# Optimization experiments

Measured on AMD Instinct MI355X. Metric: run time of the kernel, lower is better.

## Reference

```python
import jax, jax.numpy as jnp
import numpy as np

B, N, C, NH = 8, 16384, 256, 8
CH = C // NH          # head dim = 32
SCALE = CH ** -0.5
HH = WW = 128         # N = HH*WW
# CoaT crpe window dict {3:2, 5:3, 7:3}: 2 heads->3x3, 3 heads->5x5, 3 heads->7x7


def setup_inputs() -> dict:
    key = jax.random.key(0)
    ks = jax.random.split(key, 9)
    w = lambda k, shp: (jax.random.normal(k, shp, jnp.float32) * 0.02)
    return {
        "x": jax.random.normal(ks[0], (B, N, C), jnp.float32),
        "w_qkv": w(ks[1], (C, 3 * C)),              # qkv_bias=False
        "w_proj": w(ks[2], (C, C)),
        "b_proj": jnp.zeros((C,), jnp.float32),
        "w3": w(ks[3], (3, 3, 1, 2 * CH)),          # HWIO depthwise, 2 heads
        "b3": jnp.zeros((2 * CH,), jnp.float32),
        "w5": w(ks[4], (5, 5, 1, 3 * CH)),          # 3 heads
        "b5": jnp.zeros((3 * CH,), jnp.float32),
        "w7": w(ks[5], (7, 7, 1, 3 * CH)),          # 3 heads
        "b7": jnp.zeros((3 * CH,), jnp.float32),
        "H": HH,
        "W": WW,
    }


def _hydra(q, k, v):
    # q,k,v: [B, h, N, Ch]; normalize over feature dim, O(N) token reduction
    qn = q * jax.lax.rsqrt(jnp.sum(q * q, axis=-1, keepdims=True))
    kn = k * jax.lax.rsqrt(jnp.sum(k * k, axis=-1, keepdims=True))
    kv = jnp.sum(kn * v, axis=-2, keepdims=True)   # [B, h, 1, Ch]
    return qn * kv                                  # broadcast over tokens


def _dwconv(img, kern, bias):
    # img: [B, c, H, W]; kern: [kh, kw, 1, c] (HWIO depthwise)
    c = img.shape[1]
    out = jax.lax.conv_general_dilated(
        img, kern, window_strides=(1, 1), padding="SAME",
        feature_group_count=c,
        dimension_numbers=("NCHW", "HWIO", "NCHW"))
    return out + bias[None, :, None, None]


def _crpe(q, v, Hs, Ws, convs):
    # CoaT ConvRelPosEnc: depthwise conv on v per head group, gated by q
    b, h, n, ch = v.shape
    outs, idx = [], 0
    for heads, kern, bias in convs:
        vs = v[:, idx:idx + heads]                          # [B, hs, N, Ch]
        v_img = vs.transpose(0, 1, 3, 2).reshape(b, heads * ch, Hs, Ws)
        cv = _dwconv(v_img, kern, bias)
        cv = cv.reshape(b, heads, ch, n).transpose(0, 1, 3, 2)
        outs.append(q[:, idx:idx + heads] * cv)
        idx += heads
    return jnp.concatenate(outs, axis=1)                    # [B, h, N, Ch]


def reference(x, w_qkv, w_proj, b_proj, w3, b3, w5, b5, w7, b7, H, W):
    b, n, c = x.shape
    qkv = (x @ w_qkv).reshape(b, n, 3, NH, CH).transpose(2, 0, 3, 1, 4)
    q, k, v = qkv[0], qkv[1], qkv[2]                        # [B, h, N, Ch]
    factor_att = _hydra(q, k, v)
    crpe = _crpe(q, v, H, W, [(2, w3, b3), (3, w5, b5), (3, w7, b7)])
    out = SCALE * factor_att + crpe
    out = out.transpose(0, 2, 1, 3).reshape(b, n, c)        # [B, N, C]
    return out @ w_proj + b_proj
```

## Files before the change

kernel.cpp:

```cpp
#include <hip/hip_runtime.h>
#include <hip/hip_bf16.h>


typedef __hip_bfloat16 bf16;
typedef __bf16 bf16x8 __attribute__((ext_vector_type(8)));
typedef unsigned short u16x8 __attribute__((ext_vector_type(8)));
typedef float f32x4 __attribute__((ext_vector_type(4)));
typedef float f32x8 __attribute__((ext_vector_type(8)));

#define SCALE_ 0.17677669529663687f

__device__ __forceinline__ unsigned short f2b(float f) {
  __hip_bfloat16 h = __float2bfloat16(f);
  return __builtin_bit_cast(unsigned short, h);
}
__device__ __forceinline__ float blo(unsigned u) {
  return __builtin_bit_cast(float, u << 16);
}
__device__ __forceinline__ float bhi(unsigned u) {
  return __builtin_bit_cast(float, u & 0xffff0000u);
}
__device__ __forceinline__ f32x8 unpack8(uint4 u) {
  f32x8 r;
  r[0] = blo(u.x); r[1] = bhi(u.x); r[2] = blo(u.y); r[3] = bhi(u.y);
  r[4] = blo(u.z); r[5] = bhi(u.z); r[6] = blo(u.w); r[7] = bhi(u.w);
  return r;
}
__device__ __forceinline__ uint4 pack8v(const f32x8 o) {
  uint4 s;
  s.x = (unsigned)f2b(o[0]) | ((unsigned)f2b(o[1]) << 16);
  s.y = (unsigned)f2b(o[2]) | ((unsigned)f2b(o[3]) << 16);
  s.z = (unsigned)f2b(o[4]) | ((unsigned)f2b(o[5]) << 16);
  s.w = (unsigned)f2b(o[6]) | ((unsigned)f2b(o[7]) << 16);
  return s;
}
__device__ __forceinline__ void gload16(const void* g, void* l) {
  __builtin_amdgcn_global_load_lds(
      (const __attribute__((address_space(1))) unsigned int*)g,
      (__attribute__((address_space(3))) unsigned int*)l, 16, 0, 0);
}
__device__ __forceinline__ f32x4 mfma16(u16x8 a, u16x8 b, f32x4 c) {
  return __builtin_amdgcn_mfma_f32_16x16x32_bf16(
      __builtin_bit_cast(bf16x8, a), __builtin_bit_cast(bf16x8, b), c, 0, 0, 0);
}
__device__ __forceinline__ void barrier_vm4() {
  asm volatile("s_waitcnt vmcnt(4) lgkmcnt(0)" ::: "memory");
  __builtin_amdgcn_s_barrier();
  asm volatile("" ::: "memory");
}
__device__ __forceinline__ void barrier_vm0() {
  asm volatile("s_waitcnt vmcnt(0) lgkmcnt(0)" ::: "memory");
  __builtin_amdgcn_s_barrier();
  asm volatile("" ::: "memory");
}
__device__ __forceinline__ void barrier_vm8() {
  asm volatile("s_waitcnt vmcnt(8) lgkmcnt(0)" ::: "memory");
  __builtin_amdgcn_s_barrier();
  asm volatile("" ::: "memory");
}
__device__ __forceinline__ void fma8(f32x8& a, const f32x8 v, const float4 w0,
                                     const float4 w1) {
  a[0] += v[0] * w0.x; a[1] += v[1] * w0.y;
  a[2] += v[2] * w0.z; a[3] += v[3] * w0.w;
  a[4] += v[4] * w1.x; a[5] += v[5] * w1.y;
  a[6] += v[6] * w1.z; a[7] += v[7] * w1.w;
}

__global__ __launch_bounds__(256) void prep_weights(
    const float* __restrict__ wqkv, const float* __restrict__ wproj,
    bf16* __restrict__ wqkvT, bf16* __restrict__ wprojT) {
  const int idx = blockIdx.x * 256 + threadIdx.x;
  if (idx < 768 * 256) {
    const int j = idx >> 8, k = idx & 255;
    wqkvT[idx] = __float2bfloat16(wqkv[k * 768 + j]);
  }
  if (idx < 256 * 256) {
    const int j = idx >> 8, k = idx & 255;
    wprojT[idx] = __float2bfloat16(wproj[k * 256 + j]);
  }
}

__global__ __launch_bounds__(256) void qkv_mfma(
    const float* __restrict__ x, const bf16* __restrict__ wT,
    bf16* __restrict__ qO, bf16* __restrict__ kO, bf16* __restrict__ vO) {
  __shared__ __align__(16) char LDSU[32768];
  char* As = LDSU;
  char* Bs = LDSU + 16384;
  const int tid = threadIdx.x;
  const int l = tid & 63, w = tid >> 6;
  const int wr = w >> 1, wc = w & 1;

  const int lin = blockIdx.y * 6 + blockIdx.x;
  const int xcd = lin & 7, qq = lin >> 3;
  const int jt = qq % 6;
  const int ttile = xcd * 128 + qq / 6;
  const int j0 = jt << 7;
  const int t0 = ttile << 7;

  f32x4 acc[4][4];
#pragma unroll
  for (int m = 0; m < 4; ++m)
#pragma unroll
    for (int t = 0; t < 4; ++t) acc[m][t] = (f32x4){0.f, 0.f, 0.f, 0.f};

  const int arow0 = w * 16 + (l >> 2), arow1 = arow0 + 64;
  const int asl = l & 3;
  const bf16* asrc0 =
      wT + (size_t)(j0 + arow0) * 256 + ((asl ^ ((arow0 >> 1) & 3)) << 3);
  const bf16* asrc1 =
      wT + (size_t)(j0 + arow1) * 256 + ((asl ^ ((arow1 >> 1) & 3)) << 3);
  const int ad0 = w * 1024, ad1 = 4096 + w * 1024;

  const int brow = tid >> 1, bkh = tid & 1;
  const float* xp = x + (size_t)(t0 + brow) * 256 + bkh * 16;
  const int bsw = (brow >> 1) & 3;
  const int bw0 = brow * 64 + (((bkh << 1) ^ bsw) << 4);
  const int bw1 = brow * 64 + ((((bkh << 1) | 1) ^ bsw) << 4);

  const int fr = l & 15;
  const int fq = l >> 4;
  const int fs = (fq ^ ((l >> 1) & 3)) << 4;

  float4 xs[3][4];

  gload16(asrc0, As + ad0);
  gload16(asrc1, As + ad1);
#pragma unroll
  for (int s = 0; s < 3; ++s)
#pragma unroll
    for (int i = 0; i < 4; ++i)
      xs[s][i] = *(const float4*)(xp + s * 32 + i * 4);
  {
    u16x8 p0, p1;
    p0[0] = f2b(xs[0][0].x); p0[1] = f2b(xs[0][0].y);
    p0[2] = f2b(xs[0][0].z); p0[3] = f2b(xs[0][0].w);
    p0[4] = f2b(xs[0][1].x); p0[5] = f2b(xs[0][1].y);
    p0[6] = f2b(xs[0][1].z); p0[7] = f2b(xs[0][1].w);
    p1[0] = f2b(xs[0][2].x); p1[1] = f2b(xs[0][2].y);
    p1[2] = f2b(xs[0][2].z); p1[3] = f2b(xs[0][2].w);
    p1[4] = f2b(xs[0][3].x); p1[5] = f2b(xs[0][3].y);
    p1[6] = f2b(xs[0][3].z); p1[7] = f2b(xs[0][3].w);
    *(u16x8*)(Bs + bw0) = p0;
    *(u16x8*)(Bs + bw1) = p1;
  }
  barrier_vm8();

#pragma unroll
  for (int t = 0; t < 8; ++t) {
    if (t < 7) {
      const int kn = (t + 1) << 5;
      char* Adst = As + (((t + 1) & 1) << 13);
      gload16(asrc0 + kn, Adst + ad0);
      gload16(asrc1 + kn, Adst + ad1);
    }
    if (t < 5) {
#pragma unroll
      for (int i = 0; i < 4; ++i)
        xs[t % 3][i] = *(const float4*)(xp + (t + 3) * 32 + i * 4);
    }
    const char* Ac = As + ((t & 1) << 13);
    const char* Bc = Bs + ((t & 1) << 13);
    u16x8 af[4], bfv[4];
#pragma unroll
    for (int m = 0; m < 4; ++m)
      af[m] = *(const u16x8*)(Ac + (wr * 64 + m * 16 + fr) * 64 + fs);
#pragma unroll
    for (int tt = 0; tt < 4; ++tt)
      bfv[tt] = *(const u16x8*)(Bc + (wc * 64 + tt * 16 + fr) * 64 + fs);
    __builtin_amdgcn_s_setprio(1);
#pragma unroll
    for (int m = 0; m < 4; ++m)
#pragma unroll
      for (int tt = 0; tt < 4; ++tt)
        acc[m][tt] = mfma16(af[m], bfv[tt], acc[m][tt]);
    __builtin_amdgcn_s_setprio(0);
    if (t < 7) {
      const float4* xv = xs[(t + 1) % 3];
      u16x8 p0, p1;
      p0[0] = f2b(xv[0].x); p0[1] = f2b(xv[0].y);
      p0[2] = f2b(xv[0].z); p0[3] = f2b(xv[0].w);
      p0[4] = f2b(xv[1].x); p0[5] = f2b(xv[1].y);
      p0[6] = f2b(xv[1].z); p0[7] = f2b(xv[1].w);
      p1[0] = f2b(xv[2].x); p1[1] = f2b(xv[2].y);
      p1[2] = f2b(xv[2].z); p1[3] = f2b(xv[2].w);
      p1[4] = f2b(xv[3].x); p1[5] = f2b(xv[3].y);
      p1[6] = f2b(xv[3].z); p1[7] = f2b(xv[3].w);
      char* Bdst = Bs + (((t + 1) & 1) << 13);
      *(u16x8*)(Bdst + bw0) = p0;
      *(u16x8*)(Bdst + bw1) = p1;
    }
    if (t < 5) barrier_vm4();
    else if (t < 7) barrier_vm0();
  }
  __syncthreads();

#pragma unroll
  for (int m = 0; m < 4; ++m) {
    const int jq = wr * 16 + m * 4 + fq;
#pragma unroll
    for (int t = 0; t < 4; ++t) {
      const int token = wc * 64 + t * 16 + fr;
      const int p = jq ^ (token & 15);
      uint2 pk;
      pk.x = (unsigned)f2b(acc[m][t][0]) | ((unsigned)f2b(acc[m][t][1]) << 16);
      pk.y = (unsigned)f2b(acc[m][t][2]) | ((unsigned)f2b(acc[m][t][3]) << 16);
      *(uint2*)(LDSU + token * 256 + (p << 3)) = pk;
    }
  }
  __syncthreads();

  const int region = j0 >> 8;
  bf16* outp = (region == 0) ? qO : ((region == 1) ? kO : vO);
  const int b = t0 >> 14;
  const int n0 = t0 & 16383;
  const int jl = j0 & 255;
  const int seg = tid & 15;
#pragma unroll
  for (int r = 0; r < 8; ++r) {
    const int token = r * 16 + (tid >> 4);
    const int tsw = token & 15;
    const uint2 lo = *(const uint2*)(LDSU + token * 256 + (((2 * seg) ^ tsw) << 3));
    const uint2 hi =
        *(const uint2*)(LDSU + token * 256 + (((2 * seg + 1) ^ tsw) << 3));
    uint4 d;
    d.x = lo.x; d.y = lo.y; d.z = hi.x; d.w = hi.y;
    *(uint4*)&outp[((size_t)b * 16384 + n0 + token) * 256 + jl + seg * 8] = d;
  }
}

__global__ __launch_bounds__(256) void kv_reduce(
    const bf16* __restrict__ kT, const bf16* __restrict__ vT,
    float* __restrict__ kv) {
  __shared__ float red[256 * 8];
  const int tid = threadIdx.x;
  const int b = blockIdx.y;
  const int seg = tid & 31;
  f32x8 part = (f32x8)0.f;

  for (int r = 0; r < 32; ++r) {
    const int token = blockIdx.x * 256 + r * 8 + (tid >> 5);
    const size_t roff = ((size_t)b * 16384 + token) * 256;
    const uint4 kd = *(const uint4*)(kT + roff + seg * 8);
    const f32x8 kf = unpack8(kd);
    float ss = 0.f;
#pragma unroll
    for (int i = 0; i < 8; ++i) ss += kf[i] * kf[i];
    ss += __shfl_xor(ss, 1);
    ss += __shfl_xor(ss, 2);
    const float inv = rsqrtf(ss);
    const uint4 vd = *(const uint4*)(vT + roff + seg * 8);
    const f32x8 vf = unpack8(vd);
#pragma unroll
    for (int i = 0; i < 8; ++i) part[i] += kf[i] * inv * vf[i];
  }
#pragma unroll
  for (int i = 0; i < 8; ++i) red[tid * 8 + i] = part[i];
  __syncthreads();
  if (tid < 32) {
    f32x8 s = (f32x8)0.f;
#pragma unroll
    for (int k = 0; k < 8; ++k)
#pragma unroll
      for (int i = 0; i < 8; ++i) s[i] += red[(tid + 32 * k) * 8 + i];
#pragma unroll
    for (int i = 0; i < 8; ++i)
      atomicAdd(&kv[b * 256 + seg * 8 + i], s[i]);
  }
}

template <int K>
__global__ __launch_bounds__(256) void crpe_conv(
    const bf16* __restrict__ qT, const bf16* __restrict__ vT,
    const float* __restrict__ kvbuf, const float* __restrict__ wp,
    const float* __restrict__ bp, int OC, int hbase,
    bf16* __restrict__ mid) {
  constexpr int R = K / 2;
  constexpr int SY = 16 + 2 * R;
  constexpr int SXr = 32 + 2 * R;
  constexpr int SX = SXr + 1;
  constexpr int PL = SX * SY;
  __shared__ __align__(16) uint4 vs[4 * PL];
  __shared__ float wlds[K * K * 32];
  __shared__ float blds[32];

  const int tid = threadIdx.x;
  const int hg = blockIdx.x;
  const int h = hbase + hg;
  const int tile = blockIdx.y;
  const int b = blockIdx.z;
  const int tx0 = (tile & 3) * 32, ty0 = (tile >> 2) * 16;
  const int tx = tid & 15, ty = tid >> 4;
  const int ocbase = hg * 32;

  {
    const int cc = tid & 3;
    for (int e = tid >> 2; e < SXr * SY; e += 64) {
      const int ly = e / SXr, lx = e - ly * SXr;
      const int gy = ty0 - R + ly, gx = tx0 - R + lx;
      uint4 d = {0, 0, 0, 0};
      if (gy >= 0 && gy < 128 && gx >= 0 && gx < 128)
        d = *((const uint4*)(vT + ((size_t)b * 16384 + gy * 128 + gx) * 256 +
                             h * 32) + cc);
      vs[cc * PL + ly * SX + lx] = d;
    }
  }
  for (int e = tid; e < K * K * 32; e += 256)
    wlds[e] = wp[(e >> 5) * OC + ocbase + (e & 31)];
  if (tid < 32) blds[tid] = bp[ocbase + tid];
  __syncthreads();

  const int n = (ty0 + ty) * 128 + tx0 + 2 * tx;
  const size_t off0 = ((size_t)b * 16384 + n) * 256 + h * 32;
  const uint4* q0 = (const uint4*)(qT + off0);
  const uint4* q1 = (const uint4*)(qT + off0 + 256);
  float ss0 = 0.f, ss1 = 0.f;
#pragma unroll
  for (int cc = 0; cc < 4; ++cc) {
    const f32x8 a = unpack8(q0[cc]);
    const f32x8 c = unpack8(q1[cc]);
#pragma unroll
    for (int i = 0; i < 8; ++i) { ss0 += a[i] * a[i]; ss1 += c[i] * c[i]; }
  }
  const float qinv0 = rsqrtf(ss0), qinv1 = rsqrtf(ss1);
  const float4* kvp = (const float4*)(kvbuf + ((size_t)b * 8 + h) * 32);
  const float4* wlds4 = (const float4*)wlds;
  const float4* bl4 = (const float4*)blds;
  uint4* m0 = (uint4*)(mid + off0);
  uint4* m1 = (uint4*)(mid + off0 + 256);

#pragma unroll 1
  for (int cc = 0; cc < 4; ++cc) {
    const uint4* vplane = vs + cc * PL;
    const float4 ba = bl4[cc * 2], bb = bl4[cc * 2 + 1];
    f32x8 a0, a1;
    a0[0] = ba.x; a0[1] = ba.y; a0[2] = ba.z; a0[3] = ba.w;
    a0[4] = bb.x; a0[5] = bb.y; a0[6] = bb.z; a0[7] = bb.w;
    a1 = a0;
#pragma unroll
    for (int ky = 0; ky < K; ++ky) {
      const uint4* vrow = vplane + (ty + ky) * SX + 2 * tx;
      f32x8 vcur = unpack8(vrow[0]);
#pragma unroll
      for (int kx = 0; kx < K; ++kx) {
        const f32x8 vnx = unpack8(vrow[kx + 1]);
        const float4 w0 = wlds4[(ky * K + kx) * 8 + cc * 2];
        const float4 w1 = wlds4[(ky * K + kx) * 8 + cc * 2 + 1];
        fma8(a0, vcur, w0, w1);
        fma8(a1, vnx, w0, w1);
        vcur = vnx;
      }
    }
    const float4 ka = kvp[cc * 2], kb = kvp[cc * 2 + 1];
    f32x8 kvf;
    kvf[0] = ka.x; kvf[1] = ka.y; kvf[2] = ka.z; kvf[3] = ka.w;
    kvf[4] = kb.x; kvf[5] = kb.y; kvf[6] = kb.z; kvf[7] = kb.w;
    {
      const f32x8 qv = unpack8(q0[cc]);
      f32x8 o;
#pragma unroll
      for (int i = 0; i < 8; ++i)
        o[i] = SCALE_ * qv[i] * qinv0 * kvf[i] + qv[i] * a0[i];
      m0[cc] = pack8v(o);
    }
    {
      const f32x8 qv = unpack8(q1[cc]);
      f32x8 o;
#pragma unroll
      for (int i = 0; i < 8; ++i)
        o[i] = SCALE_ * qv[i] * qinv1 * kvf[i] + qv[i] * a1[i];
      m1[cc] = pack8v(o);
    }
  }
}

__global__ __launch_bounds__(256) void proj_mfma(
    const bf16* __restrict__ mid, const bf16* __restrict__ wpT,
    const float* __restrict__ bproj, float* __restrict__ out) {
  __shared__ __align__(16) char LDSU[49152];
  char* As = LDSU;
  char* Bs = LDSU + 24576;
  const int tid = threadIdx.x;
  const int l = tid & 63, w = tid >> 6;
  const int wr = w >> 1, wc = w & 1;

  const int lin = blockIdx.y * 2 + blockIdx.x;
  const int xcd = lin & 7, qq = lin >> 3;
  const int jt = qq & 1;
  const int ttile = xcd * 128 + (qq >> 1);
  const int j0 = jt << 7;
  const int tk0 = ttile << 7;

  f32x4 acc[4][4];
#pragma unroll
  for (int m = 0; m < 4; ++m)
#pragma unroll
    for (int t = 0; t < 4; ++t) acc[m][t] = (f32x4){0.f, 0.f, 0.f, 0.f};

  const int row0 = w * 16 + (l >> 2), row1 = row0 + 64;
  const int sl = l & 3;
  const int sw0 = (row0 >> 1) & 3, sw1 = (row1 >> 1) & 3;
  const bf16* asrc0 = wpT + (size_t)(j0 + row0) * 256 + ((sl ^ sw0) << 3);
  const bf16* asrc1 = wpT + (size_t)(j0 + row1) * 256 + ((sl ^ sw1) << 3);
  const bf16* bsrc0 = mid + (size_t)(tk0 + row0) * 256 + ((sl ^ sw0) << 3);
  const bf16* bsrc1 = mid + (size_t)(tk0 + row1) * 256 + ((sl ^ sw1) << 3);
  const int d0 = w * 1024, d1 = 4096 + w * 1024;

  const int fr = l & 15;
  const int fq = l >> 4;
  const int fs = (fq ^ ((l >> 1) & 3)) << 4;

  gload16(asrc0, As + d0);
  gload16(asrc1, As + d1);
  gload16(bsrc0, Bs + d0);
  gload16(bsrc1, Bs + d1);
  gload16(asrc0 + 32, As + 8192 + d0);
  gload16(asrc1 + 32, As + 8192 + d1);
  gload16(bsrc0 + 32, Bs + 8192 + d0);
  gload16(bsrc1 + 32, Bs + 8192 + d1);
  barrier_vm4();

#pragma unroll
  for (int t = 0; t < 8; ++t) {
    if (t < 6) {
      const int kn = (t + 2) << 5;
      const int nb = ((t + 2) % 3) * 8192;
      gload16(asrc0 + kn, As + nb + d0);
      gload16(asrc1 + kn, As + nb + d1);
      gload16(bsrc0 + kn, Bs + nb + d0);
      gload16(bsrc1 + kn, Bs + nb + d1);
    }
    const char* Ac = As + (t % 3) * 8192;
    const char* Bc = Bs + (t % 3) * 8192;
    u16x8 af[4], bfv[4];
#pragma unroll
    for (int m = 0; m < 4; ++m)
      af[m] = *(const u16x8*)(Ac + (wr * 64 + m * 16 + fr) * 64 + fs);
#pragma unroll
    for (int tt = 0; tt < 4; ++tt)
      bfv[tt] = *(const u16x8*)(Bc + (wc * 64 + tt * 16 + fr) * 64 + fs);
    __builtin_amdgcn_s_setprio(1);
#pragma unroll
    for (int m = 0; m < 4; ++m)
#pragma unroll
      for (int tt = 0; tt < 4; ++tt)
        acc[m][tt] = mfma16(af[m], bfv[tt], acc[m][tt]);
    __builtin_amdgcn_s_setprio(0);
    if (t < 6) barrier_vm4();
    else if (t < 7) barrier_vm0();
  }
  __syncthreads();

#pragma unroll
  for (int m = 0; m < 4; ++m) {
    const float4 bias = *(const float4*)&bproj[j0 + wr * 64 + m * 16 + fq * 4];
#pragma unroll
    for (int t = 0; t < 4; ++t) {
      acc[m][t][0] += bias.x;
      acc[m][t][1] += bias.y;
      acc[m][t][2] += bias.z;
      acc[m][t][3] += bias.w;
    }
  }

  for (int chunk = 0; chunk < 2; ++chunk) {
    if (wc == chunk) {
#pragma unroll
      for (int m = 0; m < 4; ++m) {
        const int jq = wr * 16 + m * 4 + fq;
#pragma unroll
        for (int t = 0; t < 4; ++t) {
          const int ltok = t * 16 + fr;
          const int p = jq ^ (ltok & 15);
          float4 r;
          r.x = acc[m][t][0]; r.y = acc[m][t][1];
          r.z = acc[m][t][2]; r.w = acc[m][t][3];
          *(float4*)(LDSU + ltok * 512 + (p << 4)) = r;
        }
      }
    }
    __syncthreads();
    const int seg = tid & 31;
#pragma unroll
    for (int r = 0; r < 8; ++r) {
      const int ltok = r * 8 + (tid >> 5);
      const int p = seg ^ (ltok & 15);
      const float4 dv = *(const float4*)(LDSU + ltok * 512 + (p << 4));
      *(float4*)&out[(size_t)(tk0 + chunk * 64 + ltok) * 256 + j0 + seg * 4] = dv;
    }
    __syncthreads();
  }
}

extern "C" void kernel_launch(void* const* d_in, const int* in_sizes, int n_in,
                              void* d_out, int out_size, void* d_ws,
                              size_t ws_size, hipStream_t stream) {
  const float* x     = (const float*)d_in[0];
  const float* wqkv  = (const float*)d_in[1];
  const float* wproj = (const float*)d_in[2];
  const float* bproj = (const float*)d_in[3];
  const float* w3 = (const float*)d_in[4];
  const float* b3 = (const float*)d_in[5];
  const float* w5 = (const float*)d_in[6];
  const float* b5 = (const float*)d_in[7];
  const float* w7 = (const float*)d_in[8];
  const float* b7 = (const float*)d_in[9];
  float* out = (float*)d_out;

  const size_t PLANE = (size_t)8 * 16384 * 256;
  bf16* qT  = (bf16*)d_ws;
  bf16* vT  = qT + PLANE;
  bf16* kT  = vT + PLANE;
  bf16* mid = kT;
  float* kv = (float*)(kT + PLANE);
  bf16* wqkvT  = (bf16*)(kv + 2048);
  bf16* wprojT = wqkvT + 768 * 256;

  hipMemsetAsync(kv, 0, 2048 * sizeof(float), stream);
  prep_weights<<<dim3(768), 256, 0, stream>>>(wqkv, wproj, wqkvT, wprojT);
  qkv_mfma<<<dim3(6, 1024), 256, 0, stream>>>(x, wqkvT, qT, kT, vT);
  kv_reduce<<<dim3(64, 8), 256, 0, stream>>>(kT, vT, kv);
  crpe_conv<3><<<dim3(2, 32, 8), 256, 0, stream>>>(qT, vT, kv, w3, b3, 64, 0, mid);
  crpe_conv<5><<<dim3(3, 32, 8), 256, 0, stream>>>(qT, vT, kv, w5, b5, 96, 2, mid);
  crpe_conv<7><<<dim3(3, 32, 8), 256, 0, stream>>>(qT, vT, kv, w7, b7, 96, 5, mid);
  proj_mfma<<<dim3(2, 1024), 256, 0, stream>>>(mid, wprojT, bproj, out);
}
```

Measured before the change: 381.7 us.

## Stage full activation tile in LDS, stream weights into registers, drop per-step barriers

Both the QKV and projection GEMM kernels now load the whole 128-token x 256-K activation tile into a 64KB swizzled LDS buffer up front, with an fp32-to-bf16 conversion pass in qkv and a global_load_lds copy in proj. Weight fragments are read straight from global memory into registers with a 3-deep register ring. This removes the per-K-step LDS double buffering and the barriers between steps. The projection epilogue is also changed to write all 128 tokens through LDS in a single pass instead of two chunks. The cost is 64KB of LDS per block, which lowers occupancy. Weight reads from global are also less coalesced, and the kernel no longer overlaps activation loading with MFMA work.

```diff
diff --git a/kernel.cpp b/kernel.cpp
--- a/kernel.cpp
+++ b/kernel.cpp
@@ -43,21 +43,6 @@
   return __builtin_amdgcn_mfma_f32_16x16x32_bf16(
       __builtin_bit_cast(bf16x8, a), __builtin_bit_cast(bf16x8, b), c, 0, 0, 0);
 }
-__device__ __forceinline__ void barrier_vm4() {
-  asm volatile("s_waitcnt vmcnt(4) lgkmcnt(0)" ::: "memory");
-  __builtin_amdgcn_s_barrier();
-  asm volatile("" ::: "memory");
-}
-__device__ __forceinline__ void barrier_vm0() {
-  asm volatile("s_waitcnt vmcnt(0) lgkmcnt(0)" ::: "memory");
-  __builtin_amdgcn_s_barrier();
-  asm volatile("" ::: "memory");
-}
-__device__ __forceinline__ void barrier_vm8() {
-  asm volatile("s_waitcnt vmcnt(8) lgkmcnt(0)" ::: "memory");
-  __builtin_amdgcn_s_barrier();
-  asm volatile("" ::: "memory");
-}
 __device__ __forceinline__ void fma8(f32x8& a, const f32x8 v, const float4 w0,
                                      const float4 w1) {
   a[0] += v[0] * w0.x; a[1] += v[1] * w0.y;
@@ -83,9 +68,7 @@
 __global__ __launch_bounds__(256) void qkv_mfma(
     const float* __restrict__ x, const bf16* __restrict__ wT,
     bf16* __restrict__ qO, bf16* __restrict__ kO, bf16* __restrict__ vO) {
-  __shared__ __align__(16) char LDSU[32768];
-  char* As = LDSU;
-  char* Bs = LDSU + 16384;
+  __shared__ __align__(16) char XL[65536];
   const int tid = threadIdx.x;
   const int l = tid & 63, w = tid >> 6;
   const int wr = w >> 1, wc = w & 1;
@@ -96,101 +79,71 @@
   const int ttile = xcd * 128 + qq / 6;
   const int j0 = jt << 7;
   const int t0 = ttile << 7;
-
-  f32x4 acc[4][4];
-#pragma unroll
-  for (int m = 0; m < 4; ++m)
-#pragma unroll
-    for (int t = 0; t < 4; ++t) acc[m][t] = (f32x4){0.f, 0.f, 0.f, 0.f};
-
-  const int arow0 = w * 16 + (l >> 2), arow1 = arow0 + 64;
-  const int asl = l & 3;
-  const bf16* asrc0 =
-      wT + (size_t)(j0 + arow0) * 256 + ((asl ^ ((arow0 >> 1) & 3)) << 3);
-  const bf16* asrc1 =
-      wT + (size_t)(j0 + arow1) * 256 + ((asl ^ ((arow1 >> 1) & 3)) << 3);
-  const int ad0 = w * 1024, ad1 = 4096 + w * 1024;
-
-  const int brow = tid >> 1, bkh = tid & 1;
-  const float* xp = x + (size_t)(t0 + brow) * 256 + bkh * 16;
-  const int bsw = (brow >> 1) & 3;
-  const int bw0 = brow * 64 + (((bkh << 1) ^ bsw) << 4);
-  const int bw1 = brow * 64 + ((((bkh << 1) | 1) ^ bsw) << 4);
+  const int b = t0 >> 14;
+  const int n0 = t0 & 16383;
+
+  {
+    const int tk = tid >> 5, s = tid & 31;
+#pragma unroll 4
+    for (int r = 0; r < 16; ++r) {
+      const int row = r * 8 + tk;
+      const float4 a0 = *(const float4*)(x + (size_t)(t0 + row) * 256 + s * 8);
+      const float4 a1 =
+          *(const float4*)(x + (size_t)(t0 + row) * 256 + s * 8 + 4);
+      u16x8 p;
+      p[0] = f2b(a0.x); p[1] = f2b(a0.y); p[2] = f2b(a0.z); p[3] = f2b(a0.w);
+      p[4] = f2b(a1.x); p[5] = f2b(a1.y); p[6] = f2b(a1.z); p[7] = f2b(a1.w);
+      *(u16x8*)(XL + row * 512 + ((s ^ (row & 7)) << 4)) = p;
+    }
+  }
 
   const int fr = l & 15;
   const int fq = l >> 4;
-  const int fs = (fq ^ ((l >> 1) & 3)) << 4;
-
-  float4 xs[3][4];
-
-  gload16(asrc0, As + ad0);
-  gload16(asrc1, As + ad1);
-#pragma unroll
-  for (int s = 0; s < 3; ++s)
-#pragma unroll
-    for (int i = 0; i < 4; ++i)
-      xs[s][i] = *(const float4*)(xp + s * 32 + i * 4);
-  {
-    u16x8 p0, p1;
-    p0[0] = f2b(xs[0][0].x); p0[1] = f2b(xs[0][0].y);
-    p0[2] = f2b(xs[0][0].z); p0[3] = f2b(xs[0][0].w);
-    p0[4] = f2b(xs[0][1].x); p0[5] = f2b(xs[0][1].y);
-    p0[6] = f2b(xs[0][1].z); p0[7] = f2b(xs[0][1].w);
-    p1[0] = f2b(xs[0][2].x); p1[1] = f2b(xs[0][2].y);
-    p1[2] = f2b(xs[0][2].z); p1[3] = f2b(xs[0][2].w);
-    p1[4] = f2b(xs[0][3].x); p1[5] = f2b(xs[0][3].y);
-    p1[6] = f2b(xs[0][3].z); p1[7] = f2b(xs[0][3].w);
-    *(u16x8*)(Bs + bw0) = p0;
-    *(u16x8*)(Bs + bw1) = p1;
-  }
-  barrier_vm8();
+
+  const bf16* abase = wT + (size_t)(j0 + wr * 64 + fr) * 256 + fq * 8;
+
+  int btok[4], btsw[4];
+#pragma unroll
+  for (int tt = 0; tt < 4; ++tt) {
+    btok[tt] = wc * 64 + tt * 16 + fr;
+    btsw[tt] = btok[tt] & 7;
+  }
+
+  f32x4 acc[4][4];
+#pragma unroll
+  for (int m = 0; m < 4; ++m)
+#pragma unroll
+    for (int t = 0; t < 4; ++t) acc[m][t] = (f32x4){0.f, 0.f, 0.f, 0.f};
+
+  u16x8 wreg[3][4];
+#pragma unroll
+  for (int s = 0; s < 2; ++s)
+#pragma unroll
+    for (int m = 0; m < 4; ++m)
+      wreg[s][m] = *(const u16x8*)(abase + m * 4096 + s * 32);
+
+  __syncthreads();
 
 #pragma unroll
   for (int t = 0; t < 8; ++t) {
-    if (t < 7) {
-      const int kn = (t + 1) << 5;
-      char* Adst = As + (((t + 1) & 1) << 13);
-      gload16(asrc0 + kn, Adst + ad0);
-      gload16(asrc1 + kn, Adst + ad1);
-    }
-    if (t < 5) {
-#pragma unroll
-      for (int i = 0; i < 4; ++i)
-        xs[t % 3][i] = *(const float4*)(xp + (t + 3) * 32 + i * 4);
-    }
-    const char* Ac = As + ((t & 1) << 13);
-    const char* Bc = Bs + ((t & 1) << 13);
-    u16x8 af[4], bfv[4];
+    if (t < 6) {
+#pragma unroll
+      for (int m = 0; m < 4; ++m)
+        wreg[(t + 2) % 3][m] =
+            *(const u16x8*)(abase + m * 4096 + (t + 2) * 32);
+    }
+    u16x8 bfv[4];
+#pragma unroll
+    for (int tt = 0; tt < 4; ++tt)
+      bfv[tt] = *(const u16x8*)(XL + btok[tt] * 512 +
+                                (((4 * t + fq) ^ btsw[tt]) << 4));
+    __builtin_amdgcn_s_setprio(1);
 #pragma unroll
     for (int m = 0; m < 4; ++m)
-      af[m] = *(const u16x8*)(Ac + (wr * 64 + m * 16 + fr) * 64 + fs);
-#pragma unroll
-    for (int tt = 0; tt < 4; ++tt)
-      bfv[tt] = *(const u16x8*)(Bc + (wc * 64 + tt * 16 + fr) * 64 + fs);
-    __builtin_amdgcn_s_setprio(1);
-#pragma unroll
-    for (int m = 0; m < 4; ++m)
 #pragma unroll
       for (int tt = 0; tt < 4; ++tt)
-        acc[m][tt] = mfma16(af[m], bfv[tt], acc[m][tt]);
+        acc[m][tt] = mfma16(wreg[t % 3][m], bfv[tt], acc[m][tt]);
     __builtin_amdgcn_s_setprio(0);
-    if (t < 7) {
-      const float4* xv = xs[(t + 1) % 3];
-      u16x8 p0, p1;
-      p0[0] = f2b(xv[0].x); p0[1] = f2b(xv[0].y);
-      p0[2] = f2b(xv[0].z); p0[3] = f2b(xv[0].w);
-      p0[4] = f2b(xv[1].x); p0[5] = f2b(xv[1].y);
-      p0[6] = f2b(xv[1].z); p0[7] = f2b(xv[1].w);
-      p1[0] = f2b(xv[2].x); p1[1] = f2b(xv[2].y);
-      p1[2] = f2b(xv[2].z); p1[3] = f2b(xv[2].w);
-      p1[4] = f2b(xv[3].x); p1[5] = f2b(xv[3].y);
-      p1[6] = f2b(xv[3].z); p1[7] = f2b(xv[3].w);
-      char* Bdst = Bs + (((t + 1) & 1) << 13);
-      *(u16x8*)(Bdst + bw0) = p0;
-      *(u16x8*)(Bdst + bw1) = p1;
-    }
-    if (t < 5) barrier_vm4();
-    else if (t < 7) barrier_vm0();
   }
   __syncthreads();
 
@@ -204,24 +157,22 @@
       uint2 pk;
       pk.x = (unsigned)f2b(acc[m][t][0]) | ((unsigned)f2b(acc[m][t][1]) << 16);
       pk.y = (unsigned)f2b(acc[m][t][2]) | ((unsigned)f2b(acc[m][t][3]) << 16);
-      *(uint2*)(LDSU + token * 256 + (p << 3)) = pk;
+      *(uint2*)(XL + token * 256 + (p << 3)) = pk;
     }
   }
   __syncthreads();
 
   const int region = j0 >> 8;
   bf16* outp = (region == 0) ? qO : ((region == 1) ? kO : vO);
-  const int b = t0 >> 14;
-  const int n0 = t0 & 16383;
   const int jl = j0 & 255;
   const int seg = tid & 15;
 #pragma unroll
   for (int r = 0; r < 8; ++r) {
     const int token = r * 16 + (tid >> 4);
     const int tsw = token & 15;
-    const uint2 lo = *(const uint2*)(LDSU + token * 256 + (((2 * seg) ^ tsw) << 3));
+    const uint2 lo = *(const uint2*)(XL + token * 256 + (((2 * seg) ^ tsw) << 3));
     const uint2 hi =
-        *(const uint2*)(LDSU + token * 256 + (((2 * seg + 1) ^ tsw) << 3));
+        *(const uint2*)(XL + token * 256 + (((2 * seg + 1) ^ tsw) << 3));
     uint4 d;
     d.x = lo.x; d.y = lo.y; d.z = hi.x; d.w = hi.y;
     *(uint4*)&outp[((size_t)b * 16384 + n0 + token) * 256 + jl + seg * 8] = d;
@@ -376,9 +327,7 @@
 __global__ __launch_bounds__(256) void proj_mfma(
     const bf16* __restrict__ mid, const bf16* __restrict__ wpT,
     const float* __restrict__ bproj, float* __restrict__ out) {
-  __shared__ __align__(16) char LDSU[49152];
-  char* As = LDSU;
-  char* Bs = LDSU + 24576;
+  __shared__ __align__(16) char XL[65536];
   const int tid = threadIdx.x;
   const int l = tid & 63, w = tid >> 6;
   const int wr = w >> 1, wc = w & 1;
@@ -389,66 +338,68 @@
   const int ttile = xcd * 128 + (qq >> 1);
   const int j0 = jt << 7;
   const int tk0 = ttile << 7;
-
-  f32x4 acc[4][4];
-#pragma unroll
-  for (int m = 0; m < 4; ++m)
-#pragma unroll
-    for (int t = 0; t < 4; ++t) acc[m][t] = (f32x4){0.f, 0.f, 0.f, 0.f};
-
-  const int row0 = w * 16 + (l >> 2), row1 = row0 + 64;
-  const int sl = l & 3;
-  const int sw0 = (row0 >> 1) & 3, sw1 = (row1 >> 1) & 3;
-  const bf16* asrc0 = wpT + (size_t)(j0 + row0) * 256 + ((sl ^ sw0) << 3);
-  const bf16* asrc1 = wpT + (size_t)(j0 + row1) * 256 + ((sl ^ sw1) << 3);
-  const bf16* bsrc0 = mid + (size_t)(tk0 + row0) * 256 + ((sl ^ sw0) << 3);
-  const bf16* bsrc1 = mid + (size_t)(tk0 + row1) * 256 + ((sl ^ sw1) << 3);
-  const int d0 = w * 1024, d1 = 4096 + w * 1024;
+  const int b = tk0 >> 14;
+  const int n0 = tk0 & 16383;
+
+  {
+    const int ltk = l >> 5;
+    const int s = l & 31;
+#pragma unroll 4
+    for (int i = 0; i < 16; ++i) {
+      const int shot_tok = w * 32 + i * 2;
+      const int tok = shot_tok + ltk;
+      gload16(mid + ((size_t)b * 16384 + n0 + tok) * 256 + ((s ^ (tok & 7)) << 3),
+              XL + shot_tok * 512);
+    }
+  }
 
   const int fr = l & 15;
   const int fq = l >> 4;
-  const int fs = (fq ^ ((l >> 1) & 3)) << 4;
-
-  gload16(asrc0, As + d0);
-  gload16(asrc1, As + d1);
-  gload16(bsrc0, Bs + d0);
-  gload16(bsrc1, Bs + d1);
-  gload16(asrc0 + 32, As + 8192 + d0);
-  gload16(asrc1 + 32, As + 8192 + d1);
-  gload16(bsrc0 + 32, Bs + 8192 + d0);
-  gload16(bsrc1 + 32, Bs + 8192 + d1);
-  barrier_vm4();
+  const bf16* abase = wpT + (size_t)(j0 + wr * 64 + fr) * 256 + fq * 8;
+
+  int btok[4], btsw[4];
+#pragma unroll
+  for (int tt = 0; tt < 4; ++tt) {
+    btok[tt] = wc * 64 + tt * 16 + fr;
+    btsw[tt] = btok[tt] & 7;
+  }
+
+  f32x4 acc[4][4];
+#pragma unroll
+  for (int m = 0; m < 4; ++m)
+#pragma unroll
+    for (int t = 0; t < 4; ++t) acc[m][t] = (f32x4){0.f, 0.f, 0.f, 0.f};
+
+  u16x8 wreg[3][4];
+#pragma unroll
+  for (int s = 0; s < 2; ++s)
+#pragma unroll
+    for (int m = 0; m < 4; ++m)
+      wreg[s][m] = *(const u16x8*)(abase + m * 4096 + s * 32);
+
+  __syncthreads();
 
 #pragma unroll
   for (int t = 0; t < 8; ++t) {
     if (t < 6) {
-      const int kn = (t + 2) << 5;
-      const int nb = ((t + 2) % 3) * 8192;
-      gload16(asrc0 + kn, As + nb + d0);
-      gload16(asrc1 + kn, As + nb + d1);
-      gload16(bsrc0 + kn, Bs + nb + d0);
-      gload16(bsrc1 + kn, Bs + nb + d1);
-    }
-    const char* Ac = As + (t % 3) * 8192;
-    const char* Bc = Bs + (t % 3) * 8192;
-    u16x8 af[4], bfv[4];
+#pragma unroll
+      for (int m = 0; m < 4; ++m)
+        wreg[(t + 2) % 3][m] =
+            *(const u16x8*)(abase + m * 4096 + (t + 2) * 32);
+    }
+    u16x8 bfv[4];
+#pragma unroll
+    for (int tt = 0; tt < 4; ++tt)
+      bfv[tt] = *(const u16x8*)(XL + btok[tt] * 512 +
+                                (((4 * t + fq) ^ btsw[tt]) << 4));
+    __builtin_amdgcn_s_setprio(1);
 #pragma unroll
     for (int m = 0; m < 4; ++m)
-      af[m] = *(const u16x8*)(Ac + (wr * 64 + m * 16 + fr) * 64 + fs);
-#pragma unroll
-    for (int tt = 0; tt < 4; ++tt)
-      bfv[tt] = *(const u16x8*)(Bc + (wc * 64 + tt * 16 + fr) * 64 + fs);
-    __builtin_amdgcn_s_setprio(1);
-#pragma unroll
-    for (int m = 0; m < 4; ++m)
 #pragma unroll
       for (int tt = 0; tt < 4; ++tt)
-        acc[m][tt] = mfma16(af[m], bfv[tt], acc[m][tt]);
+        acc[m][tt] = mfma16(wreg[t % 3][m], bfv[tt], acc[m][tt]);
     __builtin_amdgcn_s_setprio(0);
-    if (t < 6) barrier_vm4();
-    else if (t < 7) barrier_vm0();
-  }
-  __syncthreads();
+  }
 
 #pragma unroll
   for (int m = 0; m < 4; ++m) {
@@ -461,33 +412,29 @@
       acc[m][t][3] += bias.w;
     }
   }
-
-  for (int chunk = 0; chunk < 2; ++chunk) {
-    if (wc == chunk) {
-#pragma unroll
-      for (int m = 0; m < 4; ++m) {
-        const int jq = wr * 16 + m * 4 + fq;
-#pragma unroll
-        for (int t = 0; t < 4; ++t) {
-          const int ltok = t * 16 + fr;
-          const int p = jq ^ (ltok & 15);
-          float4 r;
-          r.x = acc[m][t][0]; r.y = acc[m][t][1];
-          r.z = acc[m][t][2]; r.w = acc[m][t][3];
-          *(float4*)(LDSU + ltok * 512 + (p << 4)) = r;
-        }
-      }
-    }
-    __syncthreads();
-    const int seg = tid & 31;
-#pragma unroll
-    for (int r = 0; r < 8; ++r) {
-      const int ltok = r * 8 + (tid >> 5);
-      const int p = seg ^ (ltok & 15);
-      const float4 dv = *(const float4*)(LDSU + ltok * 512 + (p << 4));
-      *(float4*)&out[(size_t)(tk0 + chunk * 64 + ltok) * 256 + j0 + seg * 4] = dv;
-    }
-    __syncthreads();
+  __syncthreads();
+
+#pragma unroll
+  for (int m = 0; m < 4; ++m) {
+    const int jq = wr * 16 + m * 4 + fq;
+#pragma unroll
+    for (int t = 0; t < 4; ++t) {
+      const int ltok = wc * 64 + t * 16 + fr;
+      const int p = jq ^ (ltok & 7);
+      float4 r;
+      r.x = acc[m][t][0]; r.y = acc[m][t][1];
+      r.z = acc[m][t][2]; r.w = acc[m][t][3];
+      *(float4*)(XL + ltok * 512 + (p << 4)) = r;
+    }
+  }
+  __syncthreads();
+#pragma unroll
+  for (int r = 0; r < 16; ++r) {
+    const int lin2 = r * 256 + tid;
+    const int ltok = lin2 >> 5, seg = lin2 & 31;
+    const float4 dv =
+        *(const float4*)(XL + ltok * 512 + ((seg ^ (ltok & 7)) << 4));
+    *(float4*)&out[(size_t)(tk0 + ltok) * 256 + j0 + seg * 4] = dv;
   }
 }
 
```

New measurement: 416.0 us. 1.09x slower.

## Pre-convert x to bf16 and triple-buffer both GEMM operands via direct LDS loads

Applied to the files above, without the earlier changes.

Adds a separate kernel that converts x from fp32 to bf16 into the output buffer, which serves as scratch. The QKV GEMM then streams both operands with global_load_lds into a three-stage LDS ring instead of holding fp32 x in registers and converting it inside the loop. The aim is to cut register pressure and VALU conversion work in the main loop and to prefetch two stages ahead. The cost is an extra 32M-element pass over x (read fp32, write bf16, read bf16 again) and a larger LDS allocation, which may reduce occupancy.

```diff
diff --git a/kernel.cpp b/kernel.cpp
--- a/kernel.cpp
+++ b/kernel.cpp
@@ -53,11 +53,6 @@
   __builtin_amdgcn_s_barrier();
   asm volatile("" ::: "memory");
 }
-__device__ __forceinline__ void barrier_vm8() {
-  asm volatile("s_waitcnt vmcnt(8) lgkmcnt(0)" ::: "memory");
-  __builtin_amdgcn_s_barrier();
-  asm volatile("" ::: "memory");
-}
 __device__ __forceinline__ void fma8(f32x8& a, const f32x8 v, const float4 w0,
                                      const float4 w1) {
   a[0] += v[0] * w0.x; a[1] += v[1] * w0.y;
@@ -80,12 +75,23 @@
   }
 }
 
+__global__ __launch_bounds__(256) void prep_x(const float* __restrict__ x,
+                                              bf16* __restrict__ xb) {
+  const size_t idx = ((size_t)blockIdx.x * 256 + threadIdx.x) * 8;
+  const float4 a0 = *(const float4*)(x + idx);
+  const float4 a1 = *(const float4*)(x + idx + 4);
+  u16x8 p;
+  p[0] = f2b(a0.x); p[1] = f2b(a0.y); p[2] = f2b(a0.z); p[3] = f2b(a0.w);
+  p[4] = f2b(a1.x); p[5] = f2b(a1.y); p[6] = f2b(a1.z); p[7] = f2b(a1.w);
+  *(u16x8*)(xb + idx) = p;
+}
+
 __global__ __launch_bounds__(256) void qkv_mfma(
-    const float* __restrict__ x, const bf16* __restrict__ wT,
+    const bf16* __restrict__ xb, const bf16* __restrict__ wT,
     bf16* __restrict__ qO, bf16* __restrict__ kO, bf16* __restrict__ vO) {
-  __shared__ __align__(16) char LDSU[32768];
+  __shared__ __align__(16) char LDSU[49152];
   char* As = LDSU;
-  char* Bs = LDSU + 16384;
+  char* Bs = LDSU + 24576;
   const int tid = threadIdx.x;
   const int l = tid & 63, w = tid >> 6;
   const int wr = w >> 1, wc = w & 1;
@@ -96,6 +102,8 @@
   const int ttile = xcd * 128 + qq / 6;
   const int j0 = jt << 7;
   const int t0 = ttile << 7;
+  const int b = t0 >> 14;
+  const int n0 = t0 & 16383;
 
   f32x4 acc[4][4];
 #pragma unroll
@@ -103,63 +111,41 @@
 #pragma unroll
     for (int t = 0; t < 4; ++t) acc[m][t] = (f32x4){0.f, 0.f, 0.f, 0.f};
 
-  const int arow0 = w * 16 + (l >> 2), arow1 = arow0 + 64;
-  const int asl = l & 3;
-  const bf16* asrc0 =
-      wT + (size_t)(j0 + arow0) * 256 + ((asl ^ ((arow0 >> 1) & 3)) << 3);
-  const bf16* asrc1 =
-      wT + (size_t)(j0 + arow1) * 256 + ((asl ^ ((arow1 >> 1) & 3)) << 3);
-  const int ad0 = w * 1024, ad1 = 4096 + w * 1024;
-
-  const int brow = tid >> 1, bkh = tid & 1;
-  const float* xp = x + (size_t)(t0 + brow) * 256 + bkh * 16;
-  const int bsw = (brow >> 1) & 3;
-  const int bw0 = brow * 64 + (((bkh << 1) ^ bsw) << 4);
-  const int bw1 = brow * 64 + ((((bkh << 1) | 1) ^ bsw) << 4);
+  const int row0 = w * 16 + (l >> 2), row1 = row0 + 64;
+  const int sl = l & 3;
+  const int sw0 = (row0 >> 1) & 3, sw1 = (row1 >> 1) & 3;
+  const bf16* asrc0 = wT + (size_t)(j0 + row0) * 256 + ((sl ^ sw0) << 3);
+  const bf16* asrc1 = wT + (size_t)(j0 + row1) * 256 + ((sl ^ sw1) << 3);
+  const bf16* bsrc0 = xb + (size_t)(t0 + row0) * 256 + ((sl ^ sw0) << 3);
+  const bf16* bsrc1 = xb + (size_t)(t0 + row1) * 256 + ((sl ^ sw1) << 3);
+  const int d0 = w * 1024, d1 = 4096 + w * 1024;
 
   const int fr = l & 15;
   const int fq = l >> 4;
   const int fs = (fq ^ ((l >> 1) & 3)) << 4;
 
-  float4 xs[3][4];
-
-  gload16(asrc0, As + ad0);
-  gload16(asrc1, As + ad1);
-#pragma unroll
-  for (int s = 0; s < 3; ++s)
-#pragma unroll
-    for (int i = 0; i < 4; ++i)
-      xs[s][i] = *(const float4*)(xp + s * 32 + i * 4);
-  {
-    u16x8 p0, p1;
-    p0[0] = f2b(xs[0][0].x); p0[1] = f2b(xs[0][0].y);
-    p0[2] = f2b(xs[0][0].z); p0[3] = f2b(xs[0][0].w);
-    p0[4] = f2b(xs[0][1].x); p0[5] = f2b(xs[0][1].y);
-    p0[6] = f2b(xs[0][1].z); p0[7] = f2b(xs[0][1].w);
-    p1[0] = f2b(xs[0][2].x); p1[1] = f2b(xs[0][2].y);
-    p1[2] = f2b(xs[0][2].z); p1[3] = f2b(xs[0][2].w);
-    p1[4] = f2b(xs[0][3].x); p1[5] = f2b(xs[0][3].y);
-    p1[6] = f2b(xs[0][3].z); p1[7] = f2b(xs[0][3].w);
-    *(u16x8*)(Bs + bw0) = p0;
-    *(u16x8*)(Bs + bw1) = p1;
-  }
-  barrier_vm8();
+  gload16(asrc0, As + d0);
+  gload16(asrc1, As + d1);
+  gload16(bsrc0, Bs + d0);
+  gload16(bsrc1, Bs + d1);
+  gload16(asrc0 + 32, As + 8192 + d0);
+  gload16(asrc1 + 32, As + 8192 + d1);
+  gload16(bsrc0 + 32, Bs + 8192 + d0);
+  gload16(bsrc1 + 32, Bs + 8192 + d1);
+  barrier_vm4();
 
 #pragma unroll
   for (int t = 0; t < 8; ++t) {
-    if (t < 7) {
-      const int kn = (t + 1) << 5;
-      char* Adst = As + (((t + 1) & 1) << 13);
-      gload16(asrc0 + kn, Adst + ad0);
-      gload16(asrc1 + kn, Adst + ad1);
-    }
-    if (t < 5) {
-#pragma unroll
-      for (int i = 0; i < 4; ++i)
-        xs[t % 3][i] = *(const float4*)(xp + (t + 3) * 32 + i * 4);
-    }
-    const char* Ac = As + ((t & 1) << 13);
-    const char* Bc = Bs + ((t & 1) << 13);
+    if (t < 6) {
+      const int kn = (t + 2) << 5;
+      const int nb = ((t + 2) % 3) * 8192;
+      gload16(asrc0 + kn, As + nb + d0);
+      gload16(asrc1 + kn, As + nb + d1);
+      gload16(bsrc0 + kn, Bs + nb + d0);
+      gload16(bsrc1 + kn, Bs + nb + d1);
+    }
+    const char* Ac = As + (t % 3) * 8192;
+    const char* Bc = Bs + (t % 3) * 8192;
     u16x8 af[4], bfv[4];
 #pragma unroll
     for (int m = 0; m < 4; ++m)
@@ -174,22 +160,7 @@
       for (int tt = 0; tt < 4; ++tt)
         acc[m][tt] = mfma16(af[m], bfv[tt], acc[m][tt]);
     __builtin_amdgcn_s_setprio(0);
-    if (t < 7) {
-      const float4* xv = xs[(t + 1) % 3];
-      u16x8 p0, p1;
-      p0[0] = f2b(xv[0].x); p0[1] = f2b(xv[0].y);
-      p0[2] = f2b(xv[0].z); p0[3] = f2b(xv[0].w);
-      p0[4] = f2b(xv[1].x); p0[5] = f2b(xv[1].y);
-      p0[6] = f2b(xv[1].z); p0[7] = f2b(xv[1].w);
-      p1[0] = f2b(xv[2].x); p1[1] = f2b(xv[2].y);
-      p1[2] = f2b(xv[2].z); p1[3] = f2b(xv[2].w);
-      p1[4] = f2b(xv[3].x); p1[5] = f2b(xv[3].y);
-      p1[6] = f2b(xv[3].z); p1[7] = f2b(xv[3].w);
-      char* Bdst = Bs + (((t + 1) & 1) << 13);
-      *(u16x8*)(Bdst + bw0) = p0;
-      *(u16x8*)(Bdst + bw1) = p1;
-    }
-    if (t < 5) barrier_vm4();
+    if (t < 6) barrier_vm4();
     else if (t < 7) barrier_vm0();
   }
   __syncthreads();
@@ -211,8 +182,6 @@
 
   const int region = j0 >> 8;
   bf16* outp = (region == 0) ? qO : ((region == 1) ? kO : vO);
-  const int b = t0 >> 14;
-  const int n0 = t0 & 16383;
   const int jl = j0 & 255;
   const int seg = tid & 15;
 #pragma unroll
@@ -514,10 +483,12 @@
   float* kv = (float*)(kT + PLANE);
   bf16* wqkvT  = (bf16*)(kv + 2048);
   bf16* wprojT = wqkvT + 768 * 256;
+  bf16* xb = (bf16*)d_out;
 
   hipMemsetAsync(kv, 0, 2048 * sizeof(float), stream);
   prep_weights<<<dim3(768), 256, 0, stream>>>(wqkv, wproj, wqkvT, wprojT);
-  qkv_mfma<<<dim3(6, 1024), 256, 0, stream>>>(x, wqkvT, qT, kT, vT);
+  prep_x<<<dim3(16384), 256, 0, stream>>>(x, xb);
+  qkv_mfma<<<dim3(6, 1024), 256, 0, stream>>>(xb, wqkvT, qT, kT, vT);
   kv_reduce<<<dim3(64, 8), 256, 0, stream>>>(kT, vT, kv);
   crpe_conv<3><<<dim3(2, 32, 8), 256, 0, stream>>>(qT, vT, kv, w3, b3, 64, 0, mid);
   crpe_conv<5><<<dim3(3, 32, 8), 256, 0, stream>>>(qT, vT, kv, w5, b5, 96, 2, mid);
```

Measured after the change: 353.9 us. 7.3% less time.
